# Kernel optimization log

Hardware: AMD Instinct MI355X
Metric: run time of the kernel (lower is better)

## Reference

```python
import jax, jax.numpy as jnp
import numpy as np

D_MODEL = 1024
N_HEADS_Q = 16
N_HEADS_KV = 4
D_HEAD = 64  # d_qk = d_v
THETA = 10000.0
CLAMP = 80.0


def apply_rope(x, theta=THETA):
    # x: (b, h, s, d) with d even; interleaved-pair rotary embedding
    b, h, s, d = x.shape
    inv_freq = 1.0 / (theta ** (jnp.arange(0, d, 2, dtype=jnp.float32) / d))  # (d/2,)
    ang = jnp.arange(s, dtype=jnp.float32)[:, None] * inv_freq[None, :]       # (s, d/2)
    cos, sin = jnp.cos(ang), jnp.sin(ang)
    x1, x2 = x[..., 0::2], x[..., 1::2]
    o1 = x1 * cos - x2 * sin
    o2 = x1 * sin + x2 * cos
    return jnp.stack([o1, o2], axis=-1).reshape(b, h, s, d).astype(x.dtype)


def setup_inputs() -> dict:
    key = jax.random.key(0)
    k0, k1, k2, k3, k4 = jax.random.split(key, 5)
    scale = 1.0 / np.sqrt(D_MODEL)
    return {
        "x": jax.random.normal(k0, (2, 2048, D_MODEL), dtype=jnp.float32),
        "Wq": jax.random.normal(k1, (N_HEADS_Q * D_HEAD, D_MODEL), dtype=jnp.float32) * scale,
        "Wk": jax.random.normal(k2, (N_HEADS_KV * D_HEAD, D_MODEL), dtype=jnp.float32) * scale,
        "Wv": jax.random.normal(k3, (N_HEADS_KV * D_HEAD, D_MODEL), dtype=jnp.float32) * scale,
        "Wo": jax.random.normal(k4, (D_MODEL, N_HEADS_Q * D_HEAD), dtype=jnp.float32) * scale,
    }


def _attention(x, Wq, Wk, Wv, Wo):
    b, s, _ = x.shape
    r = N_HEADS_Q // N_HEADS_KV  # queries per KV group
    # projections (Linear: y = x @ W^T, no bias)
    Q = (x @ Wq.T).reshape(b, s, N_HEADS_Q, D_HEAD).transpose(0, 2, 1, 3)   # (b, Hq, s, d)
    K = (x @ Wk.T).reshape(b, s, N_HEADS_KV, D_HEAD).transpose(0, 2, 1, 3)  # (b, Hkv, s, d)
    V = (x @ Wv.T).reshape(b, s, N_HEADS_KV, D_HEAD).transpose(0, 2, 1, 3)
    Q = apply_rope(Q)
    K = apply_rope(K)
    # GQA grouping: (b, Hkv, r, s, d)
    Qg = Q.reshape(b, N_HEADS_KV, r, s, D_HEAD)
    scores = jnp.einsum('bgrqd,bgkd->bgrqk', Qg, K)          # (b, g, r, s, s)
    scores = jnp.clip(scores, -CLAMP, CLAMP)
    causal = jnp.tril(jnp.ones((s, s), dtype=bool))
    scores = jnp.where(causal, scores, -jnp.inf)
    weights = jax.nn.softmax(scores / jnp.sqrt(jnp.float32(D_HEAD)), axis=-1)
    attn = jnp.einsum('bgrqk,bgkd->bgrqd', weights, V)       # (b, g, r, s, d)
    # '... h_kv r s d -> ... s (h_kv r d)'
    attn = attn.transpose(0, 3, 1, 2, 4).reshape(b, s, N_HEADS_Q * D_HEAD)
    return attn @ Wo.T


def reference(x, Wq, Wk, Wv, Wo):
    return _attention(x, Wq, Wk, Wv, Wo)
```

## Files before the change

kernel.cpp:

```cpp
#include <hip/hip_runtime.h>
#include <hip/hip_bf16.h>
#include <math.h>

typedef __attribute__((ext_vector_type(8))) short bf16x8;
typedef __attribute__((ext_vector_type(4))) float f32x4;

#define B_   2
#define S_   2048
#define DM   1024
#define HQ   16
#define HKV  4
#define DH   64

#define MFMA16(a, b, c) __builtin_amdgcn_mfma_f32_16x16x32_bf16(a, b, c, 0, 0, 0)

__device__ __forceinline__ void load_lds16(const __hip_bfloat16* g, __hip_bfloat16* l)
{
    __builtin_amdgcn_global_load_lds(
        (const __attribute__((address_space(1))) unsigned int*)g,
        (__attribute__((address_space(3))) unsigned int*)l, 16, 0, 0);
}

#define CVT_TOTAL 6815744
__global__ void cvt_all(const float* __restrict__ x,  const float* __restrict__ wq,
                        const float* __restrict__ wk, const float* __restrict__ wv,
                        const float* __restrict__ wo,
                        __hip_bfloat16* __restrict__ xb,  __hip_bfloat16* __restrict__ wqb,
                        __hip_bfloat16* __restrict__ wkb, __hip_bfloat16* __restrict__ wvb,
                        __hip_bfloat16* __restrict__ wob)
{
    int i = (blockIdx.x * blockDim.x + threadIdx.x) * 4;
    if (i >= CVT_TOTAL) return;
    const float* src; __hip_bfloat16* dst; int off;
    if      (i < 4194304) { src = x;  dst = xb;  off = 0; }
    else if (i < 5242880) { src = wq; dst = wqb; off = 4194304; }
    else if (i < 5505024) { src = wk; dst = wkb; off = 5242880; }
    else if (i < 5767168) { src = wv; dst = wvb; off = 5505024; }
    else                  { src = wo; dst = wob; off = 5767168; }
    i -= off;
    float4 v = *(const float4*)(src + i);
    union { ushort4 u; __hip_bfloat16 h[4]; } p;
    p.h[0] = __float2bfloat16(v.x);
    p.h[1] = __float2bfloat16(v.y);
    p.h[2] = __float2bfloat16(v.z);
    p.h[3] = __float2bfloat16(v.w);
    *(ushort4*)(dst + i) = p.u;
}

template <bool QKV>
__global__ __launch_bounds__(256, 3) void gemm_tile(
    const __hip_bfloat16* __restrict__ A,
    const __hip_bfloat16* __restrict__ W,
    float* __restrict__ C0, __hip_bfloat16* __restrict__ Qb,
    __hip_bfloat16* __restrict__ Kb, __hip_bfloat16* __restrict__ Vt, int K)
{
    const int wave = threadIdx.x >> 6;
    const int lane = threadIdx.x & 63;
    const int quad = lane >> 4;
    const int l16  = lane & 15;
    const int wm = wave >> 1, wn = wave & 1;
    const int m0 = blockIdx.x * 64;
    const int n0 = blockIdx.y * 128;

    __shared__ __align__(16) __hip_bfloat16 As[2][64 * 64];
    __shared__ __align__(16) __hip_bfloat16 Bs[2][128 * 64];

    f32x4 acc[2][4] = {};

    auto stage = [&](int sb, int kk) {
        #pragma unroll
        for (int r = 0; r < 6; ++r) {
            const int m = wave * 6 + r;
            if (m < 8) {
                const int g = (m << 6) | lane;
                const int row = g >> 3;
                const int cbs = ((g & 7) - row) & 7;
                load_lds16(A + (size_t)(m0 + row) * K + kk + cbs * 8,
                           &As[sb][m * 512]);
            } else {
                const int g = ((m - 8) << 6) | lane;
                const int row = g >> 3;
                const int cbs = ((g & 7) - row) & 7;
                load_lds16(W + (size_t)(n0 + row) * K + kk + cbs * 8,
                           &Bs[sb][(m - 8) * 512]);
            }
        }
    };

    const int NT = K >> 6;
    stage(0, 0);
    __syncthreads();

    for (int t = 0; t < NT; ++t) {
        const int buf = t & 1;
        if (t + 1 < NT) stage(buf ^ 1, (t + 1) << 6);
        #pragma unroll
        for (int ks = 0; ks < 2; ++ks) {
            bf16x8 af[2], bf[4];
            #pragma unroll
            for (int i = 0; i < 2; ++i) {
                const int ra = wm * 32 + i * 16 + l16;
                af[i] = *(const bf16x8*)
                    &As[buf][ra * 64 + ((ks * 4 + quad + ra) & 7) * 8];
            }
            #pragma unroll
            for (int j = 0; j < 4; ++j) {
                const int rb = wn * 64 + j * 16 + l16;
                bf[j] = *(const bf16x8*)
                    &Bs[buf][rb * 64 + ((ks * 4 + quad + rb) & 7) * 8];
            }
            #pragma unroll
            for (int i = 0; i < 2; ++i)
                #pragma unroll
                for (int j = 0; j < 4; ++j)
                    acc[i][j] = MFMA16(af[i], bf[j], acc[i][j]);
        }
        __syncthreads();
    }

    #pragma unroll
    for (int j = 0; j < 4; ++j) {
        const int cbase = n0 + wn * 64 + j * 16;
        const int cb = cbase + l16;
        if (QKV && cbase < 1280) {
            const int ii = (cb >> 1) & 31;
            const float f = exp2f((float)ii * -0.41524101186092f);
            const float f_rev = f * 0.15915494309189535f;
            const bool odd = cb & 1;
            #pragma unroll
            for (int i = 0; i < 2; ++i) {
                #pragma unroll
                for (int reg = 0; reg < 4; ++reg) {
                    const int row = m0 + wm * 32 + i * 16 + quad * 4 + reg;
                    const float v = acc[i][j][reg];
                    const float p = __shfl_xor(v, 1);
                    float rev = (float)(row & (S_ - 1)) * f_rev;
                    rev -= floorf(rev);
                    const float sn = __builtin_amdgcn_sinf(rev);
                    const float cs = __builtin_amdgcn_cosf(rev);
                    const float o = odd ? (p * sn + v * cs) : (v * cs - p * sn);
                    if (cbase < 1024)
                        Qb[(size_t)row * 1024 + cb] = __float2bfloat16(o);
                    else
                        Kb[(size_t)row * 256 + cb - 1024] = __float2bfloat16(o);
                }
            }
        } else {
            #pragma unroll
            for (int i = 0; i < 2; ++i) {
                #pragma unroll
                for (int reg = 0; reg < 4; ++reg) {
                    const int row = m0 + wm * 32 + i * 16 + quad * 4 + reg;
                    const float v = acc[i][j][reg];
                    if (QKV)
                        Vt[((size_t)(row >> 11) * 256 + (cb - 1280)) * S_ +
                           (row & (S_ - 1))] = __float2bfloat16(v);
                    else
                        C0[(size_t)row * 1024 + cb] = v;
                }
            }
        }
    }
}

template <bool MASKED>
__device__ __forceinline__ void softmax_store(
    const f32x4* sacc, int q, int k0, int quad, int l16,
    float& lsum, __hip_bfloat16* PsTile)
{
    #pragma unroll
    for (int nt = 0; nt < 4; ++nt) {
        union { ushort4 u; __hip_bfloat16 h[4]; } pk;
        #pragma unroll
        for (int reg = 0; reg < 4; ++reg) {
            const float sc = fminf(fmaxf(sacc[nt][reg], -80.0f), 80.0f);
            float p = exp2f(fmaf(sc, 0.18033688011112042f,
                                 -14.426950408889634f));
            if (MASKED) {
                const int key = k0 + nt * 16 + quad * 4 + reg;
                p = (key <= q) ? p : 0.0f;
            }
            lsum += p;
            pk.h[reg] = __float2bfloat16(p);
        }
        const int g = nt * 2 + (quad >> 1);
        const int s = (g + l16) & 7;
        *(ushort4*)&PsTile[l16 * 64 + s * 8 + (quad & 1) * 4] = pk.u;
    }
}

__global__ __launch_bounds__(256, 4) void attn_mfma(
    const __hip_bfloat16* __restrict__ Q,
    const __hip_bfloat16* __restrict__ K,
    const __hip_bfloat16* __restrict__ Vt,
    __hip_bfloat16* __restrict__ ctx)
{
    const int jrev = blockIdx.x >> 5;
    const int j    = 31 - jrev;
    const int bh   = blockIdx.x & 31;
    const int b    = bh >> 4;
    const int hq   = bh & 15;
    const int hkv  = hq >> 2;
    const int wave = threadIdx.x >> 6;
    const int lane = threadIdx.x & 63;
    const int quad = lane >> 4;
    const int l16  = lane & 15;

    const int q = j * 64 + wave * 16 + l16;

    __shared__ __align__(16) __hip_bfloat16 Ks[2][64 * 64];
    __shared__ __align__(16) __hip_bfloat16 Vs[2][64 * 64];
    __shared__ __align__(16) __hip_bfloat16 Ps[4][16 * 64];

    const __hip_bfloat16* qp = Q + ((size_t)(b * S_) + q) * (HQ * DH) + hq * DH + quad * 8;
    bf16x8 q0 = *(const bf16x8*)qp;
    bf16x8 q1 = *(const bf16x8*)(qp + 32);

    const __hip_bfloat16* Kg = K + (size_t)(b * S_) * (HKV * DH) + hkv * DH;
    const __hip_bfloat16* Vg = Vt + (size_t)(b * HKV + hkv) * DH * S_;

    auto stage = [&](int sb, int k0s) {
        #pragma unroll
        for (int r = 0; r < 2; ++r) {
            const int m = wave * 2 + r;
            const int g = m * 64 + lane;
            const int row = g >> 3;
            const int cbs = ((g & 7) - row) & 7;
            load_lds16(Kg + (size_t)(k0s + row) * (HKV * DH) + cbs * 8, &Ks[sb][m * 512]);
            load_lds16(Vg + (size_t)row * S_ + k0s + cbs * 8, &Vs[sb][m * 512]);
        }
    };

    stage(0, 0);

    float lsum = 0.0f;
    f32x4 O[4] = {};
    const f32x4 zro = {0.0f, 0.0f, 0.0f, 0.0f};

    for (int kt = 0; kt <= j; ++kt) {
        const int buf = kt & 1;
        const int k0 = kt * 64;
        __syncthreads();
        if (kt < j) stage(buf ^ 1, k0 + 64);

        bf16x8 ka[4][2];
        #pragma unroll
        for (int nt = 0; nt < 4; ++nt) {
            const int key = nt * 16 + l16;
            ka[nt][0] = *(const bf16x8*)&Ks[buf][key * 64 + ((quad + key) & 7) * 8];
            ka[nt][1] = *(const bf16x8*)&Ks[buf][key * 64 + ((quad + 4 + key) & 7) * 8];
        }
        f32x4 s[4];
        __builtin_amdgcn_s_setprio(1);
        #pragma unroll
        for (int nt = 0; nt < 4; ++nt) {
            s[nt] = MFMA16(ka[nt][0], q0, zro);
            s[nt] = MFMA16(ka[nt][1], q1, s[nt]);
        }
        __builtin_amdgcn_s_setprio(0);

        if (kt == j) softmax_store<true >(s, q, k0, quad, l16, lsum, &Ps[wave][0]);
        else         softmax_store<false>(s, q, k0, quad, l16, lsum, &Ps[wave][0]);
        __asm__ __volatile__("s_waitcnt lgkmcnt(0)" ::: "memory");

        bf16x8 va[2][4];
        #pragma unroll
        for (int ks = 0; ks < 2; ++ks)
            #pragma unroll
            for (int dt = 0; dt < 4; ++dt) {
                const int d = dt * 16 + l16;
                va[ks][dt] = *(const bf16x8*)
                    &Vs[buf][d * 64 + ((ks * 4 + quad + d) & 7) * 8];
            }
        __builtin_amdgcn_s_setprio(1);
        #pragma unroll
        for (int ks = 0; ks < 2; ++ks) {
            bf16x8 pb = *(const bf16x8*)
                &Ps[wave][l16 * 64 + ((ks * 4 + quad + l16) & 7) * 8];
            #pragma unroll
            for (int dt = 0; dt < 4; ++dt)
                O[dt] = MFMA16(va[ks][dt], pb, O[dt]);
        }
        __builtin_amdgcn_s_setprio(0);
    }

    lsum += __shfl_xor(lsum, 16);
    lsum += __shfl_xor(lsum, 32);
    const float inv = 1.0f / lsum;
    __hip_bfloat16* cp =
        ctx + ((size_t)(b * S_) + q) * (HQ * DH) + hq * DH + quad * 4;
    #pragma unroll
    for (int dt = 0; dt < 4; ++dt) {
        union { ushort4 u; __hip_bfloat16 h[4]; } o;
        #pragma unroll
        for (int reg = 0; reg < 4; ++reg)
            o.h[reg] = __float2bfloat16(O[dt][reg] * inv);
        *(ushort4*)(cp + dt * 16) = o.u;
    }
}

extern "C" void kernel_launch(void* const* d_in, const int* in_sizes, int n_in,
                              void* d_out, int out_size, void* d_ws, size_t ws_size,
                              hipStream_t stream)
{
    const float* x  = (const float*)d_in[0];
    const float* Wq = (const float*)d_in[1];
    const float* Wk = (const float*)d_in[2];
    const float* Wv = (const float*)d_in[3];
    const float* Wo = (const float*)d_in[4];
    float* out = (float*)d_out;

    const int M = B_ * S_;

    char* w = (char*)d_ws;
    __hip_bfloat16* xb    = (__hip_bfloat16*)w;  w += (size_t)M * DM * 2;
    __hip_bfloat16* Wqkvb = (__hip_bfloat16*)w;  w += (size_t)1536 * DM * 2;
    __hip_bfloat16* Wob   = (__hip_bfloat16*)w;  w += (size_t)DM * (HQ * DH) * 2;
    __hip_bfloat16* Qb16  = (__hip_bfloat16*)w;  w += (size_t)M * (HQ * DH) * 2;
    __hip_bfloat16* Kb16  = (__hip_bfloat16*)w;  w += (size_t)M * (HKV * DH) * 2;
    __hip_bfloat16* Vt    = (__hip_bfloat16*)w;  w += (size_t)M * (HKV * DH) * 2;
    __hip_bfloat16* ctx   = (__hip_bfloat16*)w;

    __hip_bfloat16* Wqb = Wqkvb;
    __hip_bfloat16* Wkb = Wqkvb + (size_t)1024 * 1024;
    __hip_bfloat16* Wvb = Wqkvb + (size_t)1280 * 1024;

    cvt_all<<<(CVT_TOTAL / 4 + 255) / 256, 256, 0, stream>>>(
        x, Wq, Wk, Wv, Wo, xb, Wqb, Wkb, Wvb, Wob);

    gemm_tile<true><<<dim3(M / 64, 1536 / 128), 256, 0, stream>>>(
        xb, Wqkvb, nullptr, Qb16, Kb16, Vt, DM);

    attn_mfma<<<B_ * HQ * 32, 256, 0, stream>>>(Qb16, Kb16, Vt, ctx);

    gemm_tile<false><<<dim3(M / 64, 1024 / 128), 256, 0, stream>>>(
        ctx, Wob, out, nullptr, nullptr, nullptr, HQ * DH);
}
```

Measured before the change: 160.2 us.

## Split long causal query tiles across two blocks and merge partials

Adds a chunk table so query tiles 16-31 split their key range into two blocks that write unnormalized fp32 partial outputs and row sums. A new combine kernel sums the partials and normalizes into ctx. This balances per-block work in causal attention, which had blocks with up to 32 key tiles. It costs an extra kernel launch and partial-result traffic, and reuses the output buffer as scratch.

```diff
diff --git a/kernel.cpp b/kernel.cpp
--- a/kernel.cpp
+++ b/kernel.cpp
@@ -189,18 +189,37 @@
     }
 }
 
+struct Chunk { unsigned char beg, end, j, slot; };
+__device__ __constant__ Chunk CHUNKS[48] = {
+    {0,16,15,255},{0,16,30,28},{0,16,31,30},{16,32,31,31},
+    {0,15,14,255},{0,15,28,24},{0,15,29,26},{15,30,29,27},{16,31,30,29},
+    {0,14,13,255},{0,14,26,20},{0,14,27,22},{14,28,27,23},{15,29,28,25},
+    {0,13,12,255},{0,13,24,16},{0,13,25,18},{13,26,25,19},{14,27,26,21},
+    {0,12,11,255},{0,12,22,12},{0,12,23,14},{12,24,23,15},{13,25,24,17},
+    {0,11,10,255},{0,11,20, 8},{0,11,21,10},{11,22,21,11},{12,23,22,13},
+    {0,10, 9,255},{0,10,18, 4},{0,10,19, 6},{10,20,19, 7},{11,21,20, 9},
+    {0, 9, 8,255},{0, 9,16, 0},{0, 9,17, 2},{ 9,18,17, 3},{10,19,18, 5},
+    {0, 8, 7,255},{ 9,17,16, 1},
+    {0, 7, 6,255},{0, 6, 5,255},{0, 5, 4,255},{0, 4, 3,255},
+    {0, 3, 2,255},{0, 2, 1,255},{0, 1, 0,255}
+};
+
 __global__ __launch_bounds__(256, 4) void attn_mfma(
     const __hip_bfloat16* __restrict__ Q,
     const __hip_bfloat16* __restrict__ K,
     const __hip_bfloat16* __restrict__ Vt,
-    __hip_bfloat16* __restrict__ ctx)
-{
-    const int jrev = blockIdx.x >> 5;
-    const int j    = 31 - jrev;
-    const int bh   = blockIdx.x & 31;
-    const int b    = bh >> 4;
-    const int hq   = bh & 15;
-    const int hkv  = hq >> 2;
+    __hip_bfloat16* __restrict__ ctx,
+    float* __restrict__ part,
+    float* __restrict__ lpart)
+{
+    const Chunk ck = CHUNKS[blockIdx.x >> 5];
+    const int bh  = blockIdx.x & 31;
+    const int b   = bh >> 4;
+    const int hq  = bh & 15;
+    const int hkv = hq >> 2;
+    const int j    = ck.j;
+    const int kbeg = ck.beg;
+    const int kend = ck.end;
     const int wave = threadIdx.x >> 6;
     const int lane = threadIdx.x & 63;
     const int quad = lane >> 4;
@@ -231,17 +250,17 @@
         }
     };
 
-    stage(0, 0);
+    stage(0, kbeg * 64);
 
     float lsum = 0.0f;
     f32x4 O[4] = {};
     const f32x4 zro = {0.0f, 0.0f, 0.0f, 0.0f};
 
-    for (int kt = 0; kt <= j; ++kt) {
-        const int buf = kt & 1;
+    for (int kt = kbeg; kt < kend; ++kt) {
+        const int buf = (kt - kbeg) & 1;
         const int k0 = kt * 64;
         __syncthreads();
-        if (kt < j) stage(buf ^ 1, k0 + 64);
+        if (kt + 1 < kend) stage(buf ^ 1, k0 + 64);
 
         bf16x8 ka[4][2];
         #pragma unroll
@@ -286,16 +305,61 @@
 
     lsum += __shfl_xor(lsum, 16);
     lsum += __shfl_xor(lsum, 32);
-    const float inv = 1.0f / lsum;
-    __hip_bfloat16* cp =
-        ctx + ((size_t)(b * S_) + q) * (HQ * DH) + hq * DH + quad * 4;
+
+    if (ck.slot == 255) {
+        const float inv = 1.0f / lsum;
+        __hip_bfloat16* cp =
+            ctx + ((size_t)(b * S_) + q) * (HQ * DH) + hq * DH + quad * 4;
+        #pragma unroll
+        for (int dt = 0; dt < 4; ++dt) {
+            union { ushort4 u; __hip_bfloat16 h[4]; } o;
+            #pragma unroll
+            for (int reg = 0; reg < 4; ++reg)
+                o.h[reg] = __float2bfloat16(O[dt][reg] * inv);
+            *(ushort4*)(cp + dt * 16) = o.u;
+        }
+    } else {
+        const int gslot = bh * 32 + ck.slot;
+        float* pb_ = part + (size_t)gslot * 4096 + (wave * 16 + l16) * 64 + quad * 4;
+        #pragma unroll
+        for (int dt = 0; dt < 4; ++dt) {
+            float4 v = { O[dt][0], O[dt][1], O[dt][2], O[dt][3] };
+            *(float4*)(pb_ + dt * 16) = v;
+        }
+        if (quad == 0)
+            lpart[gslot * 64 + wave * 16 + l16] = lsum;
+    }
+}
+
+__global__ __launch_bounds__(256) void attn_combine(
+    const float* __restrict__ part, const float* __restrict__ lpart,
+    __hip_bfloat16* __restrict__ ctx)
+{
+    const int bh = blockIdx.x >> 4;
+    const int jj = 16 + (blockIdx.x & 15);
+    const int b  = bh >> 4;
+    const int hq = bh & 15;
+    const int s0 = bh * 32 + (jj - 16) * 2;
+    const float4* p0 = (const float4*)(part + (size_t)s0 * 4096);
+    const float4* p1 = (const float4*)(part + (size_t)(s0 + 1) * 4096);
+    const float* l0 = lpart + s0 * 64;
+    const float* l1 = l0 + 64;
+
     #pragma unroll
-    for (int dt = 0; dt < 4; ++dt) {
+    for (int i = 0; i < 4; ++i) {
+        const int fid = i * 256 + threadIdx.x;
+        const int qr  = fid >> 4;
+        const int d4  = (fid & 15) * 4;
+        float4 a = p0[fid];
+        float4 c = p1[fid];
+        const float inv = 1.0f / (l0[qr] + l1[qr]);
         union { ushort4 u; __hip_bfloat16 h[4]; } o;
-        #pragma unroll
-        for (int reg = 0; reg < 4; ++reg)
-            o.h[reg] = __float2bfloat16(O[dt][reg] * inv);
-        *(ushort4*)(cp + dt * 16) = o.u;
+        o.h[0] = __float2bfloat16((a.x + c.x) * inv);
+        o.h[1] = __float2bfloat16((a.y + c.y) * inv);
+        o.h[2] = __float2bfloat16((a.z + c.z) * inv);
+        o.h[3] = __float2bfloat16((a.w + c.w) * inv);
+        *(ushort4*)(ctx + ((size_t)(b * S_) + jj * 64 + qr) * (HQ * DH)
+                        + hq * DH + d4) = o.u;
     }
 }
 
@@ -319,19 +383,24 @@
     __hip_bfloat16* Qb16  = (__hip_bfloat16*)w;  w += (size_t)M * (HQ * DH) * 2;
     __hip_bfloat16* Kb16  = (__hip_bfloat16*)w;  w += (size_t)M * (HKV * DH) * 2;
     __hip_bfloat16* Vt    = (__hip_bfloat16*)w;  w += (size_t)M * (HKV * DH) * 2;
-    __hip_bfloat16* ctx   = (__hip_bfloat16*)w;
+    __hip_bfloat16* ctx   = (__hip_bfloat16*)w;  w += (size_t)M * (HQ * DH) * 2;
+    float*          lpart = (float*)w;
 
     __hip_bfloat16* Wqb = Wqkvb;
     __hip_bfloat16* Wkb = Wqkvb + (size_t)1024 * 1024;
     __hip_bfloat16* Wvb = Wqkvb + (size_t)1280 * 1024;
 
+    float* part = out;
+
     cvt_all<<<(CVT_TOTAL / 4 + 255) / 256, 256, 0, stream>>>(
         x, Wq, Wk, Wv, Wo, xb, Wqb, Wkb, Wvb, Wob);
 
     gemm_tile<true><<<dim3(M / 64, 1536 / 128), 256, 0, stream>>>(
         xb, Wqkvb, nullptr, Qb16, Kb16, Vt, DM);
 
-    attn_mfma<<<B_ * HQ * 32, 256, 0, stream>>>(Qb16, Kb16, Vt, ctx);
+    attn_mfma<<<48 * 32, 256, 0, stream>>>(Qb16, Kb16, Vt, ctx, part, lpart);
+
+    attn_combine<<<512, 256, 0, stream>>>(part, lpart, ctx);
 
     gemm_tile<false><<<dim3(M / 64, 1024 / 128), 256, 0, stream>>>(
         ctx, Wob, out, nullptr, nullptr, nullptr, HQ * DH);
```

Measured after the change: 165.1 us. +3.0%, slower.

## Redistribute softmax probabilities via lane shuffles instead of LDS round-trip

Applied to the files above, without the earlier changes.

The P tile no longer goes through a per-wave LDS buffer. The probabilities are packed to bf16 in registers and moved into the MFMA B-operand layout with cross-lane shuffles, which removes the LDS store, the lgkmcnt wait and the reload. LDS addresses for K, V and the staging pointers are also precomputed outside the loop, and the masked final tile is peeled off. The cost is many ds_bpermute shuffles per tile, which also go through the LDS crossbar, plus more registers.

```diff
diff --git a/kernel.cpp b/kernel.cpp
--- a/kernel.cpp
+++ b/kernel.cpp
@@ -163,40 +163,13 @@
     }
 }
 
-template <bool MASKED>
-__device__ __forceinline__ void softmax_store(
-    const f32x4* sacc, int q, int k0, int quad, int l16,
-    float& lsum, __hip_bfloat16* PsTile)
-{
-    #pragma unroll
-    for (int nt = 0; nt < 4; ++nt) {
-        union { ushort4 u; __hip_bfloat16 h[4]; } pk;
-        #pragma unroll
-        for (int reg = 0; reg < 4; ++reg) {
-            const float sc = fminf(fmaxf(sacc[nt][reg], -80.0f), 80.0f);
-            float p = exp2f(fmaf(sc, 0.18033688011112042f,
-                                 -14.426950408889634f));
-            if (MASKED) {
-                const int key = k0 + nt * 16 + quad * 4 + reg;
-                p = (key <= q) ? p : 0.0f;
-            }
-            lsum += p;
-            pk.h[reg] = __float2bfloat16(p);
-        }
-        const int g = nt * 2 + (quad >> 1);
-        const int s = (g + l16) & 7;
-        *(ushort4*)&PsTile[l16 * 64 + s * 8 + (quad & 1) * 4] = pk.u;
-    }
-}
-
 __global__ __launch_bounds__(256, 4) void attn_mfma(
     const __hip_bfloat16* __restrict__ Q,
     const __hip_bfloat16* __restrict__ K,
     const __hip_bfloat16* __restrict__ Vt,
     __hip_bfloat16* __restrict__ ctx)
 {
-    const int jrev = blockIdx.x >> 5;
-    const int j    = 31 - jrev;
+    const int j    = 31 - (blockIdx.x >> 5);
     const int bh   = blockIdx.x & 31;
     const int b    = bh >> 4;
     const int hq   = bh & 15;
@@ -210,7 +183,6 @@
 
     __shared__ __align__(16) __hip_bfloat16 Ks[2][64 * 64];
     __shared__ __align__(16) __hip_bfloat16 Vs[2][64 * 64];
-    __shared__ __align__(16) __hip_bfloat16 Ps[4][16 * 64];
 
     const __hip_bfloat16* qp = Q + ((size_t)(b * S_) + q) * (HQ * DH) + hq * DH + quad * 8;
     bf16x8 q0 = *(const bf16x8*)qp;
@@ -219,17 +191,46 @@
     const __hip_bfloat16* Kg = K + (size_t)(b * S_) * (HKV * DH) + hkv * DH;
     const __hip_bfloat16* Vg = Vt + (size_t)(b * HKV + hkv) * DH * S_;
 
+    const __hip_bfloat16* kSrc[2]; const __hip_bfloat16* vSrc[2];
+    __hip_bfloat16* kDst[2]; __hip_bfloat16* vDst[2];
+    #pragma unroll
+    for (int r = 0; r < 2; ++r) {
+        const int m = wave * 2 + r;
+        const int g = m * 64 + lane;
+        const int row = g >> 3;
+        const int cbs = ((g & 7) - row) & 7;
+        kSrc[r] = Kg + row * (HKV * DH) + cbs * 8;
+        vSrc[r] = Vg + (size_t)row * S_ + cbs * 8;
+        kDst[r] = &Ks[0][m * 512];
+        vDst[r] = &Vs[0][m * 512];
+    }
     auto stage = [&](int sb, int k0s) {
         #pragma unroll
         for (int r = 0; r < 2; ++r) {
-            const int m = wave * 2 + r;
-            const int g = m * 64 + lane;
-            const int row = g >> 3;
-            const int cbs = ((g & 7) - row) & 7;
-            load_lds16(Kg + (size_t)(k0s + row) * (HKV * DH) + cbs * 8, &Ks[sb][m * 512]);
-            load_lds16(Vg + (size_t)row * S_ + k0s + cbs * 8, &Vs[sb][m * 512]);
+            load_lds16(kSrc[r] + k0s * (HKV * DH), kDst[r] + sb * 4096);
+            load_lds16(vSrc[r] + k0s,              vDst[r] + sb * 4096);
         }
     };
+
+    int kaoffB[4][2];
+    #pragma unroll
+    for (int nt = 0; nt < 4; ++nt)
+        #pragma unroll
+        for (int h = 0; h < 2; ++h) {
+            const int key = nt * 16 + l16;
+            kaoffB[nt][h] = (key * 64 + ((quad + 4 * h + key) & 7) * 8) * 2;
+        }
+    int vaoffB[2][4];
+    #pragma unroll
+    for (int ks = 0; ks < 2; ++ks)
+        #pragma unroll
+        for (int dt = 0; dt < 4; ++dt) {
+            const int d = dt * 16 + l16;
+            vaoffB[ks][dt] = (d * 64 + ((ks * 4 + quad + d) & 7) * 8) * 2;
+        }
+    const int srcA = (quad & 1) * 32 + l16;
+    const int srcB = srcA + 16;
+    const bool hiNT = (quad >> 1) != 0;
 
     stage(0, 0);
 
@@ -237,18 +238,20 @@
     f32x4 O[4] = {};
     const f32x4 zro = {0.0f, 0.0f, 0.0f, 0.0f};
 
-    for (int kt = 0; kt <= j; ++kt) {
+    auto body = [&](int kt, bool masked) {
         const int buf = kt & 1;
         const int k0 = kt * 64;
         __syncthreads();
         if (kt < j) stage(buf ^ 1, k0 + 64);
 
+        const char* kb = (const char*)(&Ks[0][0]) + (buf << 13);
+        const char* vb = (const char*)(&Vs[0][0]) + (buf << 13);
+
         bf16x8 ka[4][2];
         #pragma unroll
         for (int nt = 0; nt < 4; ++nt) {
-            const int key = nt * 16 + l16;
-            ka[nt][0] = *(const bf16x8*)&Ks[buf][key * 64 + ((quad + key) & 7) * 8];
-            ka[nt][1] = *(const bf16x8*)&Ks[buf][key * 64 + ((quad + 4 + key) & 7) * 8];
+            ka[nt][0] = *(const bf16x8*)(kb + kaoffB[nt][0]);
+            ka[nt][1] = *(const bf16x8*)(kb + kaoffB[nt][1]);
         }
         f32x4 s[4];
         __builtin_amdgcn_s_setprio(1);
@@ -259,30 +262,64 @@
         }
         __builtin_amdgcn_s_setprio(0);
 
-        if (kt == j) softmax_store<true >(s, q, k0, quad, l16, lsum, &Ps[wave][0]);
-        else         softmax_store<false>(s, q, k0, quad, l16, lsum, &Ps[wave][0]);
-        __asm__ __volatile__("s_waitcnt lgkmcnt(0)" ::: "memory");
+        unsigned int u[4][2];
+        #pragma unroll
+        for (int nt = 0; nt < 4; ++nt) {
+            float pv[4];
+            #pragma unroll
+            for (int reg = 0; reg < 4; ++reg) {
+                const float sc = fminf(fmaxf(s[nt][reg], -80.0f), 80.0f);
+                float x = exp2f(fmaf(sc, 0.18033688011112042f,
+                                     -14.426950408889634f));
+                if (masked && (k0 + nt * 16 + quad * 4 + reg) > q) x = 0.0f;
+                lsum += x;
+                pv[reg] = x;
+            }
+            union { unsigned short us[2]; unsigned int w; } p0, p1;
+            p0.us[0] = __bfloat16_as_ushort(__float2bfloat16(pv[0]));
+            p0.us[1] = __bfloat16_as_ushort(__float2bfloat16(pv[1]));
+            p1.us[0] = __bfloat16_as_ushort(__float2bfloat16(pv[2]));
+            p1.us[1] = __bfloat16_as_ushort(__float2bfloat16(pv[3]));
+            u[nt][0] = p0.w;
+            u[nt][1] = p1.w;
+        }
+
+        bf16x8 pbf[2];
+        #pragma unroll
+        for (int ks = 0; ks < 2; ++ks) {
+            const unsigned int a0 = __shfl((int)u[ks * 2][0],     srcA);
+            const unsigned int b0 = __shfl((int)u[ks * 2 + 1][0], srcA);
+            const unsigned int a1 = __shfl((int)u[ks * 2][1],     srcA);
+            const unsigned int b1 = __shfl((int)u[ks * 2 + 1][1], srcA);
+            const unsigned int a2 = __shfl((int)u[ks * 2][0],     srcB);
+            const unsigned int b2 = __shfl((int)u[ks * 2 + 1][0], srcB);
+            const unsigned int a3 = __shfl((int)u[ks * 2][1],     srcB);
+            const unsigned int b3 = __shfl((int)u[ks * 2 + 1][1], srcB);
+            union { unsigned int w[4]; bf16x8 v; } pk;
+            pk.w[0] = hiNT ? b0 : a0;
+            pk.w[1] = hiNT ? b1 : a1;
+            pk.w[2] = hiNT ? b2 : a2;
+            pk.w[3] = hiNT ? b3 : a3;
+            pbf[ks] = pk.v;
+        }
 
         bf16x8 va[2][4];
         #pragma unroll
         for (int ks = 0; ks < 2; ++ks)
             #pragma unroll
-            for (int dt = 0; dt < 4; ++dt) {
-                const int d = dt * 16 + l16;
-                va[ks][dt] = *(const bf16x8*)
-                    &Vs[buf][d * 64 + ((ks * 4 + quad + d) & 7) * 8];
-            }
+            for (int dt = 0; dt < 4; ++dt)
+                va[ks][dt] = *(const bf16x8*)(vb + vaoffB[ks][dt]);
         __builtin_amdgcn_s_setprio(1);
         #pragma unroll
-        for (int ks = 0; ks < 2; ++ks) {
-            bf16x8 pb = *(const bf16x8*)
-                &Ps[wave][l16 * 64 + ((ks * 4 + quad + l16) & 7) * 8];
+        for (int ks = 0; ks < 2; ++ks)
             #pragma unroll
             for (int dt = 0; dt < 4; ++dt)
-                O[dt] = MFMA16(va[ks][dt], pb, O[dt]);
-        }
+                O[dt] = MFMA16(va[ks][dt], pbf[ks], O[dt]);
         __builtin_amdgcn_s_setprio(0);
-    }
+    };
+
+    for (int kt = 0; kt < j; ++kt) body(kt, false);
+    body(j, true);
 
     lsum += __shfl_xor(lsum, 16);
     lsum += __shfl_xor(lsum, 32);
```

After: 166.6 us. 1.04x slower.

## Process two query heads per attention block to share K/V tiles across GQA group

Applied to the files above, without the earlier changes.

Each attention block now handles two query heads of the same KV group instead of one, so each staged K and V tile feeds twice as many MFMAs and the grid is halved. LDS address offsets are precomputed outside the loop and the masked diagonal tile is peeled out of the main loop. This cuts K/V global-to-LDS traffic and staging overhead per unit of work. In exchange it raises register and LDS use (occupancy hint lowered from 4 to 3) and halves the number of blocks, which may hurt load balance across CUs.

```diff
diff --git a/kernel.cpp b/kernel.cpp
--- a/kernel.cpp
+++ b/kernel.cpp
@@ -189,18 +189,17 @@
     }
 }
 
-__global__ __launch_bounds__(256, 4) void attn_mfma(
+__global__ __launch_bounds__(256, 3) void attn_mfma(
     const __hip_bfloat16* __restrict__ Q,
     const __hip_bfloat16* __restrict__ K,
     const __hip_bfloat16* __restrict__ Vt,
     __hip_bfloat16* __restrict__ ctx)
 {
-    const int jrev = blockIdx.x >> 5;
-    const int j    = 31 - jrev;
-    const int bh   = blockIdx.x & 31;
-    const int b    = bh >> 4;
-    const int hq   = bh & 15;
-    const int hkv  = hq >> 2;
+    const int j    = 31 - (blockIdx.x >> 4);
+    const int bp   = blockIdx.x & 15;
+    const int b    = bp >> 3;
+    const int hkv  = (bp >> 1) & 3;
+    const int hq0  = hkv * 4 + (bp & 1) * 2;
     const int wave = threadIdx.x >> 6;
     const int lane = threadIdx.x & 63;
     const int quad = lane >> 4;
@@ -210,93 +209,141 @@
 
     __shared__ __align__(16) __hip_bfloat16 Ks[2][64 * 64];
     __shared__ __align__(16) __hip_bfloat16 Vs[2][64 * 64];
-    __shared__ __align__(16) __hip_bfloat16 Ps[4][16 * 64];
-
-    const __hip_bfloat16* qp = Q + ((size_t)(b * S_) + q) * (HQ * DH) + hq * DH + quad * 8;
-    bf16x8 q0 = *(const bf16x8*)qp;
-    bf16x8 q1 = *(const bf16x8*)(qp + 32);
+    __shared__ __align__(16) __hip_bfloat16 Ps[4][2][16 * 64];
+
+    const __hip_bfloat16* qp =
+        Q + ((size_t)(b * S_) + q) * (HQ * DH) + hq0 * DH + quad * 8;
+    bf16x8 qA0 = *(const bf16x8*)qp;
+    bf16x8 qA1 = *(const bf16x8*)(qp + 32);
+    bf16x8 qB0 = *(const bf16x8*)(qp + 64);
+    bf16x8 qB1 = *(const bf16x8*)(qp + 96);
 
     const __hip_bfloat16* Kg = K + (size_t)(b * S_) * (HKV * DH) + hkv * DH;
     const __hip_bfloat16* Vg = Vt + (size_t)(b * HKV + hkv) * DH * S_;
 
+    const __hip_bfloat16* kSrc[2]; const __hip_bfloat16* vSrc[2];
+    __hip_bfloat16* kDst[2]; __hip_bfloat16* vDst[2];
+    #pragma unroll
+    for (int r = 0; r < 2; ++r) {
+        const int m = wave * 2 + r;
+        const int g = m * 64 + lane;
+        const int row = g >> 3;
+        const int cbs = ((g & 7) - row) & 7;
+        kSrc[r] = Kg + row * (HKV * DH) + cbs * 8;
+        vSrc[r] = Vg + (size_t)row * S_ + cbs * 8;
+        kDst[r] = &Ks[0][m * 512];
+        vDst[r] = &Vs[0][m * 512];
+    }
     auto stage = [&](int sb, int k0s) {
         #pragma unroll
         for (int r = 0; r < 2; ++r) {
-            const int m = wave * 2 + r;
-            const int g = m * 64 + lane;
-            const int row = g >> 3;
-            const int cbs = ((g & 7) - row) & 7;
-            load_lds16(Kg + (size_t)(k0s + row) * (HKV * DH) + cbs * 8, &Ks[sb][m * 512]);
-            load_lds16(Vg + (size_t)row * S_ + k0s + cbs * 8, &Vs[sb][m * 512]);
+            load_lds16(kSrc[r] + k0s * (HKV * DH), kDst[r] + sb * 4096);
+            load_lds16(vSrc[r] + k0s,              vDst[r] + sb * 4096);
         }
     };
 
+    int kaoffB[4][2];
+    #pragma unroll
+    for (int nt = 0; nt < 4; ++nt)
+        #pragma unroll
+        for (int h = 0; h < 2; ++h) {
+            const int key = nt * 16 + l16;
+            kaoffB[nt][h] = (key * 64 + ((quad + 4 * h + key) & 7) * 8) * 2;
+        }
+    int vaoffB[2][4];
+    #pragma unroll
+    for (int ks = 0; ks < 2; ++ks)
+        #pragma unroll
+        for (int dt = 0; dt < 4; ++dt) {
+            const int d = dt * 16 + l16;
+            vaoffB[ks][dt] = (d * 64 + ((ks * 4 + quad + d) & 7) * 8) * 2;
+        }
+    int pboffB[2];
+    #pragma unroll
+    for (int ks = 0; ks < 2; ++ks)
+        pboffB[ks] = (l16 * 64 + ((ks * 4 + quad + l16) & 7) * 8) * 2;
+
     stage(0, 0);
 
-    float lsum = 0.0f;
-    f32x4 O[4] = {};
+    float lsumA = 0.0f, lsumB = 0.0f;
+    f32x4 OA[4] = {}, OB[4] = {};
     const f32x4 zro = {0.0f, 0.0f, 0.0f, 0.0f};
 
-    for (int kt = 0; kt <= j; ++kt) {
+    auto body = [&](int kt, bool masked) {
         const int buf = kt & 1;
         const int k0 = kt * 64;
         __syncthreads();
         if (kt < j) stage(buf ^ 1, k0 + 64);
 
+        const char* kb = (const char*)(&Ks[0][0]) + (buf << 13);
+        const char* vb = (const char*)(&Vs[0][0]) + (buf << 13);
+
         bf16x8 ka[4][2];
         #pragma unroll
         for (int nt = 0; nt < 4; ++nt) {
-            const int key = nt * 16 + l16;
-            ka[nt][0] = *(const bf16x8*)&Ks[buf][key * 64 + ((quad + key) & 7) * 8];
-            ka[nt][1] = *(const bf16x8*)&Ks[buf][key * 64 + ((quad + 4 + key) & 7) * 8];
-        }
-        f32x4 s[4];
+            ka[nt][0] = *(const bf16x8*)(kb + kaoffB[nt][0]);
+            ka[nt][1] = *(const bf16x8*)(kb + kaoffB[nt][1]);
+        }
+        f32x4 sA[4], sB[4];
         __builtin_amdgcn_s_setprio(1);
         #pragma unroll
         for (int nt = 0; nt < 4; ++nt) {
-            s[nt] = MFMA16(ka[nt][0], q0, zro);
-            s[nt] = MFMA16(ka[nt][1], q1, s[nt]);
+            sA[nt] = MFMA16(ka[nt][0], qA0, zro);
+            sA[nt] = MFMA16(ka[nt][1], qA1, sA[nt]);
+            sB[nt] = MFMA16(ka[nt][0], qB0, zro);
+            sB[nt] = MFMA16(ka[nt][1], qB1, sB[nt]);
         }
         __builtin_amdgcn_s_setprio(0);
 
-        if (kt == j) softmax_store<true >(s, q, k0, quad, l16, lsum, &Ps[wave][0]);
-        else         softmax_store<false>(s, q, k0, quad, l16, lsum, &Ps[wave][0]);
+        if (masked) {
+            softmax_store<true >(sA, q, k0, quad, l16, lsumA, &Ps[wave][0][0]);
+            softmax_store<true >(sB, q, k0, quad, l16, lsumB, &Ps[wave][1][0]);
+        } else {
+            softmax_store<false>(sA, q, k0, quad, l16, lsumA, &Ps[wave][0][0]);
+            softmax_store<false>(sB, q, k0, quad, l16, lsumB, &Ps[wave][1][0]);
+        }
         __asm__ __volatile__("s_waitcnt lgkmcnt(0)" ::: "memory");
 
         bf16x8 va[2][4];
         #pragma unroll
         for (int ks = 0; ks < 2; ++ks)
             #pragma unroll
+            for (int dt = 0; dt < 4; ++dt)
+                va[ks][dt] = *(const bf16x8*)(vb + vaoffB[ks][dt]);
+        __builtin_amdgcn_s_setprio(1);
+        #pragma unroll
+        for (int ks = 0; ks < 2; ++ks) {
+            bf16x8 pbA = *(const bf16x8*)((const char*)&Ps[wave][0][0] + pboffB[ks]);
+            bf16x8 pbB = *(const bf16x8*)((const char*)&Ps[wave][1][0] + pboffB[ks]);
+            #pragma unroll
             for (int dt = 0; dt < 4; ++dt) {
-                const int d = dt * 16 + l16;
-                va[ks][dt] = *(const bf16x8*)
-                    &Vs[buf][d * 64 + ((ks * 4 + quad + d) & 7) * 8];
-            }
-        __builtin_amdgcn_s_setprio(1);
-        #pragma unroll
-        for (int ks = 0; ks < 2; ++ks) {
-            bf16x8 pb = *(const bf16x8*)
-                &Ps[wave][l16 * 64 + ((ks * 4 + quad + l16) & 7) * 8];
-            #pragma unroll
-            for (int dt = 0; dt < 4; ++dt)
-                O[dt] = MFMA16(va[ks][dt], pb, O[dt]);
+                OA[dt] = MFMA16(va[ks][dt], pbA, OA[dt]);
+                OB[dt] = MFMA16(va[ks][dt], pbB, OB[dt]);
+            }
         }
         __builtin_amdgcn_s_setprio(0);
-    }
-
-    lsum += __shfl_xor(lsum, 16);
-    lsum += __shfl_xor(lsum, 32);
-    const float inv = 1.0f / lsum;
-    __hip_bfloat16* cp =
-        ctx + ((size_t)(b * S_) + q) * (HQ * DH) + hq * DH + quad * 4;
-    #pragma unroll
-    for (int dt = 0; dt < 4; ++dt) {
-        union { ushort4 u; __hip_bfloat16 h[4]; } o;
-        #pragma unroll
-        for (int reg = 0; reg < 4; ++reg)
-            o.h[reg] = __float2bfloat16(O[dt][reg] * inv);
-        *(ushort4*)(cp + dt * 16) = o.u;
-    }
+    };
+
+    for (int kt = 0; kt < j; ++kt) body(kt, false);
+    body(j, true);
+
+    auto finish = [&](float lsum, const f32x4* O, int h) {
+        lsum += __shfl_xor(lsum, 16);
+        lsum += __shfl_xor(lsum, 32);
+        const float inv = 1.0f / lsum;
+        __hip_bfloat16* cp = ctx + ((size_t)(b * S_) + q) * (HQ * DH)
+                                 + (hq0 + h) * DH + quad * 4;
+        #pragma unroll
+        for (int dt = 0; dt < 4; ++dt) {
+            union { ushort4 u; __hip_bfloat16 h4[4]; } o;
+            #pragma unroll
+            for (int reg = 0; reg < 4; ++reg)
+                o.h4[reg] = __float2bfloat16(O[dt][reg] * inv);
+            *(ushort4*)(cp + dt * 16) = o.u;
+        }
+    };
+    finish(lsumA, OA, 0);
+    finish(lsumB, OB, 1);
 }
 
 extern "C" void kernel_launch(void* const* d_in, const int* in_sizes, int n_in,
@@ -331,7 +378,7 @@
     gemm_tile<true><<<dim3(M / 64, 1536 / 128), 256, 0, stream>>>(
         xb, Wqkvb, nullptr, Qb16, Kb16, Vt, DM);
 
-    attn_mfma<<<B_ * HQ * 32, 256, 0, stream>>>(Qb16, Kb16, Vt, ctx);
+    attn_mfma<<<B_ * HKV * 2 * 32, 256, 0, stream>>>(Qb16, Kb16, Vt, ctx);
 
     gemm_tile<false><<<dim3(M / 64, 1024 / 128), 256, 0, stream>>>(
         ctx, Wob, out, nullptr, nullptr, nullptr, HQ * DH);
```

New measurement: 175.4 us. 1.09x slower.
